# Optimization experiments

Measured on AMD Instinct MI355X. Metric: run time of the kernel, lower is better.

Reference implementation:

```python
import jax, jax.numpy as jnp
import numpy as np

GRID = 64            # volume_pixel per axis
VOX = 1.0 / GRID     # voxel_physical (unit-cube volume_physical)
CHUNK = 128          # gaussians per scan step


def _voxel_centers():
    # [V,3] centers of voxels of a unit cube, V = GRID**3
    c = (jnp.arange(GRID, dtype=jnp.float32) + 0.5) * VOX
    zz, yy, xx = jnp.meshgrid(c, c, c, indexing='ij')
    return jnp.stack([xx.ravel(), yy.ravel(), zz.ravel()], axis=-1)


def _quat_to_rotmat(q):
    # q: [N,4] (w,x,y,z), normalized -> [N,3,3]
    q = q / jnp.linalg.norm(q, axis=-1, keepdims=True)
    w, x, y, z = q[:, 0], q[:, 1], q[:, 2], q[:, 3]
    return jnp.stack([
        jnp.stack([1 - 2 * (y * y + z * z), 2 * (x * y - w * z), 2 * (x * z + w * y)], -1),
        jnp.stack([2 * (x * y + w * z), 1 - 2 * (x * x + z * z), 2 * (y * z - w * x)], -1),
        jnp.stack([2 * (x * z - w * y), 2 * (y * z + w * x), 1 - 2 * (x * x + y * y)], -1),
    ], axis=-2)


def _voxelize(means3D, densities, scales, rotations):
    N = means3D.shape[0]
    R = _quat_to_rotmat(rotations)                       # [N,3,3]
    inv_s2 = 1.0 / (scales * scales)                     # [N,3]
    # Sigma^{-1} = R diag(1/s^2) R^T
    Sinv = jnp.einsum('nij,nj,nkj->nik', R, inv_s2, R)   # [N,3,3]
    centers = _voxel_centers()                            # [V,3]
    n_chunks = N // CHUNK
    mu_c = means3D.reshape(n_chunks, CHUNK, 3)
    de_c = densities.reshape(n_chunks, CHUNK)
    Si_c = Sinv.reshape(n_chunks, CHUNK, 3, 3)

    def step(vol, xs):
        mu, dens, Si = xs
        d = centers[None, :, :] - mu[:, None, :]                 # [C,V,3]
        qf = jnp.einsum('cvi,cij,cvj->cv', d, Si, d)             # [C,V]
        vol = vol + jnp.sum(dens[:, None] * jnp.exp(-0.5 * qf), axis=0)
        return vol, None

    vol0 = jnp.zeros((GRID ** 3,), dtype=means3D.dtype)
    volume, _ = jax.lax.scan(step, vol0, (mu_c, de_c, Si_c))
    volume = volume.reshape(GRID, GRID, GRID)
    # screen-space-style radius: 3 sigma of the largest axis, in voxels
    radii = jnp.ceil(3.0 * jnp.max(scales, axis=-1) / VOX).astype(jnp.int32)
    return volume, radii


def setup_inputs() -> dict:
    key = jax.random.key(0)
    k1, k2, k3, k4 = jax.random.split(key, 4)
    N = 4096
    means3D = jax.random.uniform(k1, (N, 3), dtype=jnp.float32)                 # in unit cube
    densities = jax.random.uniform(k2, (N,), dtype=jnp.float32)
    scales = jax.random.uniform(k3, (N, 3), dtype=jnp.float32) * 0.05 + 0.01    # 0.6-3.8 voxels
    rotations = jax.random.normal(k4, (N, 4), dtype=jnp.float32)
    return {"means3D": means3D, "densities": densities, "scales": scales, "rotations": rotations}


def reference(means3D, densities, scales, rotations):
    return _voxelize(means3D, densities, scales, rotations)
```

## Files before the change

kernel.cpp:

```cpp
#include <hip/hip_runtime.h>

#define GRIDN 64
#define NVOX (GRIDN * GRIDN * GRIDN)
#define VOXF (1.0f / 64.0f)
#define QCUT 16.0f
#define EXPSCL (-0.72134752044f)
#define SKIPTH (QCUT * EXPSCL)

#define WS_CULLA 0
#define WS_CULLB (4 * 4096)
#define WS_REC   (8 * 4096)

__global__ __launch_bounds__(256) void prep_kernel(
    const float* __restrict__ means, const float* __restrict__ dens,
    const float* __restrict__ scales, const float* __restrict__ rots,
    float* __restrict__ ws, float* __restrict__ radii_out, int N)
{
    int i = blockIdx.x * 256 + threadIdx.x;
    if (i >= N) return;

    float qw = rots[i * 4 + 0], qx = rots[i * 4 + 1];
    float qy = rots[i * 4 + 2], qz = rots[i * 4 + 3];
    float inm = rsqrtf(qw * qw + qx * qx + qy * qy + qz * qz);
    qw *= inm; qx *= inm; qy *= inm; qz *= inm;
    float r00 = 1.f - 2.f * (qy * qy + qz * qz);
    float r01 = 2.f * (qx * qy - qw * qz);
    float r02 = 2.f * (qx * qz + qw * qy);
    float r10 = 2.f * (qx * qy + qw * qz);
    float r11 = 1.f - 2.f * (qx * qx + qz * qz);
    float r12 = 2.f * (qy * qz - qw * qx);
    float r20 = 2.f * (qx * qz - qw * qy);
    float r21 = 2.f * (qy * qz + qw * qx);
    float r22 = 1.f - 2.f * (qx * qx + qy * qy);

    float s0 = scales[i * 3 + 0], s1 = scales[i * 3 + 1], s2 = scales[i * 3 + 2];
    float v0 = s0 * s0, v1 = s1 * s1, v2 = s2 * s2;
    float i0 = 1.f / v0, i1 = 1.f / v1, i2 = 1.f / v2;

    float A = (r00 * r00 * i0 + r01 * r01 * i1 + r02 * r02 * i2) * EXPSCL;
    float B = (r10 * r10 * i0 + r11 * r11 * i1 + r12 * r12 * i2) * EXPSCL;
    float C = (r20 * r20 * i0 + r21 * r21 * i1 + r22 * r22 * i2) * EXPSCL;
    float D = (r00 * r10 * i0 + r01 * r11 * i1 + r02 * r12 * i2) * EXPSCL;
    float E = (r00 * r20 * i0 + r01 * r21 * i1 + r02 * r22 * i2) * EXPSCL;
    float F = (r10 * r20 * i0 + r11 * r21 * i1 + r12 * r22 * i2) * EXPSCL;

    float Cxx = r00 * r00 * v0 + r01 * r01 * v1 + r02 * r02 * v2;
    float Cyy = r10 * r10 * v0 + r11 * r11 * v1 + r12 * r12 * v2;
    float Czz = r20 * r20 * v0 + r21 * r21 * v1 + r22 * r22 * v2;

    float de = fmaxf(dens[i], 1e-30f);
    float qeff = fmaxf(QCUT + 2.0f * logf(de), 0.0f);
    float smax2 = fmaxf(v0, fmaxf(v1, v2));

    float mx = means[i * 3 + 0], my = means[i * 3 + 1], mz = means[i * 3 + 2];
    float4 ca; ca.x = mx; ca.y = my; ca.z = mz; ca.w = sqrtf(qeff * Cxx);
    float4 cb; cb.x = sqrtf(qeff * Cyy); cb.y = sqrtf(qeff * Czz);
    cb.z = qeff * smax2; cb.w = 0.f;
    ((float4*)(ws + WS_CULLA))[i] = ca;
    ((float4*)(ws + WS_CULLB))[i] = cb;

    float4* R = (float4*)(ws + WS_REC + (size_t)i * 16);
    float4 w0; w0.x = A; w0.y = B; w0.z = C; w0.w = 2.f * D;
    float4 w1; w1.x = 2.f * E; w1.y = 2.f * F; w1.z = -0.25f / A; w1.w = log2f(de);
    float4 w2; w2.x = mx; w2.y = my; w2.z = mz; w2.w = 0.f;
    R[0] = w0; R[1] = w1; R[2] = w2;

    float m = fmaxf(s0, fmaxf(s1, s2));
    radii_out[i] = ceilf(m * 3.0f * 64.0f);

    if (i == 0) {
        float4 zv; zv.x = 0.f; zv.y = 0.f; zv.z = 0.f; zv.w = 0.f;
        float4 d1; d1.x = 0.f; d1.y = 0.f; d1.z = 0.f; d1.w = -1e30f;
        float4* Dm = (float4*)(ws + WS_REC + (size_t)N * 16);
        Dm[0] = zv; Dm[1] = d1; Dm[2] = zv;
    }
}

#define BODY8(v0_, v1_, v2_) do {                                             \
    float dy = py - v2_.y, dz = pz - v2_.z;                                   \
    float tt  = fmaf(v1_.y, dy, v0_.z * dz);                                  \
    float qyz = fmaf(v0_.y * dy, dy, fmaf(tt, dz, v1_.w));                    \
    float gx  = fmaf(v0_.w, dy, v1_.x * dz);                                  \
    float qmx = fmaf(gx * gx, v1_.z, qyz);        \
    if (!__all(qmx < SKIPTH)) {                                               \
        float dx0 = px - v2_.x;                                               \
        float dx1 = dx0 + VOXF,        dx2 = dx0 + 2.f * VOXF;                \
        float dx3 = dx0 + 3.f * VOXF,  dx4 = dx0 + 4.f * VOXF;                \
        float dx5 = dx0 + 5.f * VOXF,  dx6 = dx0 + 6.f * VOXF;                \
        float dx7 = dx0 + 7.f * VOXF;                                         \
        accL.x += __builtin_amdgcn_exp2f(fmaf(dx0, fmaf(v0_.x, dx0, gx), qyz));\
        accL.y += __builtin_amdgcn_exp2f(fmaf(dx1, fmaf(v0_.x, dx1, gx), qyz));\
        accL.z += __builtin_amdgcn_exp2f(fmaf(dx2, fmaf(v0_.x, dx2, gx), qyz));\
        accL.w += __builtin_amdgcn_exp2f(fmaf(dx3, fmaf(v0_.x, dx3, gx), qyz));\
        accH.x += __builtin_amdgcn_exp2f(fmaf(dx4, fmaf(v0_.x, dx4, gx), qyz));\
        accH.y += __builtin_amdgcn_exp2f(fmaf(dx5, fmaf(v0_.x, dx5, gx), qyz));\
        accH.z += __builtin_amdgcn_exp2f(fmaf(dx6, fmaf(v0_.x, dx6, gx), qyz));\
        accH.w += __builtin_amdgcn_exp2f(fmaf(dx7, fmaf(v0_.x, dx7, gx), qyz));\
    }                                                                         \
} while (0)

__global__ __launch_bounds__(1024, 8) void vox_kernel(
    const float* __restrict__ ws, float* __restrict__ out, int N)
{
    __shared__ unsigned long long cmask[64];
    __shared__ int slist[3072];
    __shared__ float4 plds[16][64];

    const float* rec = ws + WS_REC;
    const int tid = threadIdx.x;
    const int lane = tid & 63, wave = tid >> 6;
    const int t = (blockIdx.x * 341) & 511;
    const int tX = t & 7, tY = (t >> 3) & 7, tZ = t >> 6;
    const int x0 = tX << 3;
    const int y = (tY << 3) + (lane & 7);
    const int z = (tZ << 3) + (lane >> 3);
    const float px = (x0 + 0.5f) * VOXF;
    const float py = (y + 0.5f) * VOXF;
    const float pz = (z + 0.5f) * VOXF;

    const float lox = (x0 + 0.5f) * VOXF,          hix = (x0 + 7.5f) * VOXF;
    const float loy = ((tY << 3) + 0.5f) * VOXF,   hiy = ((tY << 3) + 7.5f) * VOXF;
    const float loz = ((tZ << 3) + 0.5f) * VOXF,   hiz = ((tZ << 3) + 7.5f) * VOXF;

    const int nch = (N + 63) >> 6;
    #pragma unroll
    for (int k = 0; k < 4; ++k) {
        const int c = (k << 4) | wave;
        unsigned long long bal = 0ull;
        if (c < nch) {
            const int gi = (c << 6) + lane;
            const int gc = gi < N ? gi : N - 1;
            float4 ca = ((const float4*)(ws + WS_CULLA))[gc];
            float4 cb = ((const float4*)(ws + WS_CULLB))[gc];
            float cx = fminf(fmaxf(ca.x, lox), hix) - ca.x;
            float cy = fminf(fmaxf(ca.y, loy), hiy) - ca.y;
            float cz = fminf(fmaxf(ca.z, loz), hiz) - ca.z;
            float d2 = fmaf(cx, cx, fmaf(cy, cy, cz * cz));
            bool keep = (gi < N) && (d2 <= cb.z)
                && (ca.x + ca.w >= lox) && (ca.x - ca.w <= hix)
                && (ca.y + cb.x >= loy) && (ca.y - cb.x <= hiy)
                && (ca.z + cb.y >= loz) && (ca.z - cb.y <= hiz);
            bal = __ballot(keep);
        }
        if (lane == 0) cmask[c] = bal;
    }
    __syncthreads();

    unsigned long long mk = cmask[lane];
    int pc = __popcll(mk);
    int incl = pc;
    #pragma unroll
    for (int d = 1; d < 64; d <<= 1) {
        int t2 = __shfl_up(incl, d, 64);
        if (lane >= d) incl += t2;
    }
    const int excl = incl - pc;
    int cnt = __builtin_amdgcn_readlane(incl, 63);
    if (cnt > 3072) cnt = 3072;

    #pragma unroll
    for (int k = 0; k < 4; ++k) {
        const int c = (k << 4) | wave;
        unsigned long long mc = cmask[c];
        if (mc == 0ull) continue;
        int bse = __builtin_amdgcn_readlane(excl, c);
        if ((mc >> lane) & 1ull) {
            int pre = __popcll(mc & ((1ull << lane) - 1ull));
            int pos = bse + pre;
            if (pos < 3072) slist[pos] = (c << 6) + lane;
        }
    }

    int L = (((cnt + 63) >> 6) + 0) << 2;
    if (L << 4 > 3072) L = 192;
    const int padend = L << 4;
    for (int i = cnt + tid; i < padend; i += 1024) slist[i] = N;
    __syncthreads();

    float4 accL, accH;
    accL.x = accL.y = accL.z = accL.w = 0.f;
    accH = accL;

    const int beg = wave * L, end = beg + L;
    for (int base = beg; base < end; base += 64) {
        int src = base + lane;
        int vidx = slist[src < padend ? src : padend - 1];
        int m = end - base; if (m > 64) m = 64;
        for (int j = 0; j < m; j += 4) {
            int i0 = __builtin_amdgcn_readlane(vidx, j);
            int i1 = __builtin_amdgcn_readlane(vidx, j + 1);
            int i2 = __builtin_amdgcn_readlane(vidx, j + 2);
            int i3 = __builtin_amdgcn_readlane(vidx, j + 3);
            const float4* P0 = (const float4*)(rec + ((size_t)i0 << 4));
            const float4* P1 = (const float4*)(rec + ((size_t)i1 << 4));
            const float4* P2 = (const float4*)(rec + ((size_t)i2 << 4));
            const float4* P3 = (const float4*)(rec + ((size_t)i3 << 4));
            float4 a0 = P0[0], a1 = P0[1], a2 = P0[2];
            float4 b0 = P1[0], b1 = P1[1], b2 = P1[2];
            float4 c0 = P2[0], c1 = P2[1], c2 = P2[2];
            float4 d0 = P3[0], d1 = P3[1], d2 = P3[2];
            BODY8(a0, a1, a2);
            BODY8(b0, b1, b2);
            BODY8(c0, c1, c2);
            BODY8(d0, d1, d2);
        }
    }

    const int v = (z << 12) + (y << 6) + x0;

    plds[wave][lane] = accL;
    __syncthreads();
    if (wave == 0) {
        float4 r = plds[0][lane];
        #pragma unroll
        for (int w = 1; w < 16; ++w) {
            float4 p = plds[w][lane];
            r.x += p.x; r.y += p.y; r.z += p.z; r.w += p.w;
        }
        *(float4*)&out[v] = r;
    }
    __syncthreads();
    plds[wave][lane] = accH;
    __syncthreads();
    if (wave == 0) {
        float4 r = plds[0][lane];
        #pragma unroll
        for (int w = 1; w < 16; ++w) {
            float4 p = plds[w][lane];
            r.x += p.x; r.y += p.y; r.z += p.z; r.w += p.w;
        }
        *(float4*)&out[v + 4] = r;
    }
}

extern "C" void kernel_launch(void* const* d_in, const int* in_sizes, int n_in,
                              void* d_out, int out_size, void* d_ws, size_t ws_size,
                              hipStream_t stream)
{
    const float* means  = (const float*)d_in[0];
    const float* dens   = (const float*)d_in[1];
    const float* scales = (const float*)d_in[2];
    const float* rots   = (const float*)d_in[3];
    float* out = (float*)d_out;
    float* ws  = (float*)d_ws;
    const int N = in_sizes[1];

    prep_kernel<<<(N + 255) / 256, 256, 0, stream>>>(means, dens, scales, rots,
                                                     ws, out + NVOX, N);
    vox_kernel<<<512, 1024, 0, stream>>>(ws, out, N);
}
```

Baseline: 27.63 us.

## Tighten Gaussian cutoff, drop per-Gaussian wave skip, split list exactly per wave

Lowers the quadratic-form cutoff used for culling from 16 to 12, which shrinks the per-tile candidate list. Removes the wave-uniform early-out test inside the inner loop, so every candidate is evaluated unconditionally. Replaces the padded dummy-Gaussian scheme with an exact per-wave split of the list plus a scalar remainder loop. The smaller cutoff drops contributions below roughly exp(-6), which adds approximation error against the reference.

```diff
diff --git a/kernel.cpp b/kernel.cpp
--- a/kernel.cpp
+++ b/kernel.cpp
@@ -3,9 +3,8 @@
 #define GRIDN 64
 #define NVOX (GRIDN * GRIDN * GRIDN)
 #define VOXF (1.0f / 64.0f)
-#define QCUT 16.0f
+#define QCUT 12.0f
 #define EXPSCL (-0.72134752044f)
-#define SKIPTH (QCUT * EXPSCL)
 
 #define WS_CULLA 0
 #define WS_CULLB (4 * 4096)
@@ -67,13 +66,6 @@
 
     float m = fmaxf(s0, fmaxf(s1, s2));
     radii_out[i] = ceilf(m * 3.0f * 64.0f);
-
-    if (i == 0) {
-        float4 zv; zv.x = 0.f; zv.y = 0.f; zv.z = 0.f; zv.w = 0.f;
-        float4 d1; d1.x = 0.f; d1.y = 0.f; d1.z = 0.f; d1.w = -1e30f;
-        float4* Dm = (float4*)(ws + WS_REC + (size_t)N * 16);
-        Dm[0] = zv; Dm[1] = d1; Dm[2] = zv;
-    }
 }
 
 #define BODY8(v0_, v1_, v2_) do {                                             \
@@ -81,22 +73,19 @@
     float tt  = fmaf(v1_.y, dy, v0_.z * dz);                                  \
     float qyz = fmaf(v0_.y * dy, dy, fmaf(tt, dz, v1_.w));                    \
     float gx  = fmaf(v0_.w, dy, v1_.x * dz);                                  \
-    float qmx = fmaf(gx * gx, v1_.z, qyz);        \
-    if (!__all(qmx < SKIPTH)) {                                               \
-        float dx0 = px - v2_.x;                                               \
-        float dx1 = dx0 + VOXF,        dx2 = dx0 + 2.f * VOXF;                \
-        float dx3 = dx0 + 3.f * VOXF,  dx4 = dx0 + 4.f * VOXF;                \
-        float dx5 = dx0 + 5.f * VOXF,  dx6 = dx0 + 6.f * VOXF;                \
-        float dx7 = dx0 + 7.f * VOXF;                                         \
-        accL.x += __builtin_amdgcn_exp2f(fmaf(dx0, fmaf(v0_.x, dx0, gx), qyz));\
-        accL.y += __builtin_amdgcn_exp2f(fmaf(dx1, fmaf(v0_.x, dx1, gx), qyz));\
-        accL.z += __builtin_amdgcn_exp2f(fmaf(dx2, fmaf(v0_.x, dx2, gx), qyz));\
-        accL.w += __builtin_amdgcn_exp2f(fmaf(dx3, fmaf(v0_.x, dx3, gx), qyz));\
-        accH.x += __builtin_amdgcn_exp2f(fmaf(dx4, fmaf(v0_.x, dx4, gx), qyz));\
-        accH.y += __builtin_amdgcn_exp2f(fmaf(dx5, fmaf(v0_.x, dx5, gx), qyz));\
-        accH.z += __builtin_amdgcn_exp2f(fmaf(dx6, fmaf(v0_.x, dx6, gx), qyz));\
-        accH.w += __builtin_amdgcn_exp2f(fmaf(dx7, fmaf(v0_.x, dx7, gx), qyz));\
-    }                                                                         \
+    float dx0 = px - v2_.x;                                                   \
+    float dx1 = dx0 + VOXF,        dx2 = dx0 + 2.f * VOXF;                    \
+    float dx3 = dx0 + 3.f * VOXF,  dx4 = dx0 + 4.f * VOXF;                    \
+    float dx5 = dx0 + 5.f * VOXF,  dx6 = dx0 + 6.f * VOXF;                    \
+    float dx7 = dx0 + 7.f * VOXF;                                             \
+    accL.x += __builtin_amdgcn_exp2f(fmaf(dx0, fmaf(v0_.x, dx0, gx), qyz));   \
+    accL.y += __builtin_amdgcn_exp2f(fmaf(dx1, fmaf(v0_.x, dx1, gx), qyz));   \
+    accL.z += __builtin_amdgcn_exp2f(fmaf(dx2, fmaf(v0_.x, dx2, gx), qyz));   \
+    accL.w += __builtin_amdgcn_exp2f(fmaf(dx3, fmaf(v0_.x, dx3, gx), qyz));   \
+    accH.x += __builtin_amdgcn_exp2f(fmaf(dx4, fmaf(v0_.x, dx4, gx), qyz));   \
+    accH.y += __builtin_amdgcn_exp2f(fmaf(dx5, fmaf(v0_.x, dx5, gx), qyz));   \
+    accH.z += __builtin_amdgcn_exp2f(fmaf(dx6, fmaf(v0_.x, dx6, gx), qyz));   \
+    accH.w += __builtin_amdgcn_exp2f(fmaf(dx7, fmaf(v0_.x, dx7, gx), qyz));   \
 } while (0)
 
 __global__ __launch_bounds__(1024, 8) void vox_kernel(
@@ -170,23 +159,20 @@
             if (pos < 3072) slist[pos] = (c << 6) + lane;
         }
     }
-
-    int L = (((cnt + 63) >> 6) + 0) << 2;
-    if (L << 4 > 3072) L = 192;
-    const int padend = L << 4;
-    for (int i = cnt + tid; i < padend; i += 1024) slist[i] = N;
     __syncthreads();
 
     float4 accL, accH;
     accL.x = accL.y = accL.z = accL.w = 0.f;
     accH = accL;
 
-    const int beg = wave * L, end = beg + L;
+    const int beg = (wave * cnt) >> 4;
+    const int end = ((wave + 1) * cnt) >> 4;
     for (int base = beg; base < end; base += 64) {
         int src = base + lane;
-        int vidx = slist[src < padend ? src : padend - 1];
+        int vidx = slist[src < cnt ? src : cnt - 1];
         int m = end - base; if (m > 64) m = 64;
-        for (int j = 0; j < m; j += 4) {
+        int j = 0;
+        for (; j + 4 <= m; j += 4) {
             int i0 = __builtin_amdgcn_readlane(vidx, j);
             int i1 = __builtin_amdgcn_readlane(vidx, j + 1);
             int i2 = __builtin_amdgcn_readlane(vidx, j + 2);
@@ -204,6 +190,12 @@
             BODY8(c0, c1, c2);
             BODY8(d0, d1, d2);
         }
+        for (; j < m; ++j) {
+            int i0 = __builtin_amdgcn_readlane(vidx, j);
+            const float4* P0 = (const float4*)(rec + ((size_t)i0 << 4));
+            float4 a0 = P0[0], a1 = P0[1], a2 = P0[2];
+            BODY8(a0, a1, a2);
+        }
     }
 
     const int v = (z << 12) + (y << 6) + x0;
```

Result: faster. 25.62 us (-7.3%).
